# Optimization experiments

Hardware: AMD Instinct MI355X
Metric: run time of the kernel (lower is better)

The kernel has to match this reference:

```python
import jax, jax.numpy as jnp
import numpy as np

B, S = 8, 512          # batch, seq_len
D, F = 1024, 2048      # d_model, head hidden dim
H = 16                 # num_tasks (= num heads)
V = 3000               # selfies vocab
O = 1                  # head output size
INIT = 0.02


def setup_inputs() -> dict:
    key = jax.random.key(0)
    ks = jax.random.split(key, 12)
    return {
        "selfies": jax.random.randint(ks[0], (B, S), 0, V),
        "tasks": jax.random.randint(ks[1], (B, S), 0, H + 1),  # 0 -> invalid (-1)
        "values": jax.random.normal(ks[2], (B, S), jnp.float32),
        "property_mask": jax.random.randint(ks[3], (B, S), 0, 2).astype(bool),
        # shared_base params (embed + FFN -> [B,S,D])
        "emb_selfies": jax.random.normal(ks[4], (V, D), jnp.float32) * INIT,
        "emb_tasks": jax.random.normal(ks[5], (H + 1, D), jnp.float32) * INIT,
        "val_vec": jax.random.normal(ks[6], (D,), jnp.float32) * INIT,
        "Ws": jax.random.normal(ks[7], (D, D), jnp.float32) * INIT,
        "bs": jnp.zeros((D,), jnp.float32),
        # stacked per-head MLP params: Linear(D,F) -> GELU -> Linear(F,O)
        "W1": jax.random.normal(ks[8], (H, D, F), jnp.float32) * INIT,
        "b1": jnp.zeros((H, F), jnp.float32),
        "W2": jax.random.normal(ks[9], (H, F, O), jnp.float32) * INIT,
        "b2": jnp.zeros((H, O), jnp.float32),
    }


def reference(selfies, tasks, values, property_mask,
              emb_selfies, emb_tasks, val_vec, Ws, bs, W1, b1, W2, b2):
    # ---- shared_base: embed + masked token features + FFN -> [B,S,D] ----
    h = (emb_selfies[selfies] + emb_tasks[tasks] + values[..., None] * val_vec)
    h = h * property_mask[..., None].astype(h.dtype)
    shared = jax.nn.gelu(h @ Ws + bs)                      # [B,S,D]

    # ---- routing: task token -> head index, 0 means invalid (-1) ----
    head_idx = jnp.where(tasks > 0, (tasks - 1) % H, -1)   # [B,S]

    # ---- each active head runs its MLP over the FULL shared_output ----
    hid = jax.nn.gelu(jnp.einsum('bsd,hdf->bshf', shared, W1) + b1)  # [B,S,H,F]
    heads_out = jnp.einsum('bshf,hfo->bsho', hid, W2) + b2           # [B,S,H,O]

    # ---- scatter/select per token by head index; invalid -> zeros ----
    idx = jnp.clip(head_idx, 0)
    out = jnp.take_along_axis(heads_out, idx[..., None, None], axis=2)[:, :, 0, :]
    return jnp.where(head_idx[..., None] >= 0, out, jnp.zeros_like(out))
```

## Files before the change

### kernel.cpp

```cpp
#include <hip/hip_runtime.h>
#include <hip/hip_bf16.h>

#define TOK 4096
#define DD  1024
#define FF  2048
#define NH  16

typedef short bf16x8 __attribute__((ext_vector_type(8)));
typedef float f32x4  __attribute__((ext_vector_type(4)));

__device__ __forceinline__ float gelu_f(float x) {
  float u = 0.7978845608028654f * (x + 0.044715f * x * x * x);
  float e = __expf(2.0f * u);
  return 0.5f * x * (2.0f - 2.0f / (e + 1.0f));
}

__device__ __forceinline__ unsigned short f2bf(float f) {
  union { float f; unsigned u; } v; v.f = f;
  unsigned r = v.u + 0x7FFF + ((v.u >> 16) & 1);
  return (unsigned short)(r >> 16);
}
__device__ __forceinline__ unsigned pack2(float a, float b) {
  return (unsigned)f2bf(a) | ((unsigned)f2bf(b) << 16);
}

__device__ __forceinline__ void load_lds16(const void* g, void* l) {
  __builtin_amdgcn_global_load_lds(
      (const __attribute__((address_space(1))) void*)g,
      (__attribute__((address_space(3))) void*)l, 16, 0, 0);
}

__device__ __forceinline__ void wtile_convert(
    const float* __restrict__ src, int stride,
    unsigned short* __restrict__ dstBase, int nt0, int kc0,
    unsigned short (*T)[70]) {
  const int tid = threadIdx.x;
  {
    int r = tid >> 2, cq = (tid & 3) * 16;
    const float* p = src + (size_t)r * stride + cq;
#pragma unroll
    for (int i = 0; i < 4; ++i) {
      float4 v = *(const float4*)(p + i * 4);
      *(unsigned*)&T[r][cq + i * 4 + 0] = pack2(v.x, v.y);
      *(unsigned*)&T[r][cq + i * 4 + 2] = pack2(v.z, v.w);
    }
  }
  __syncthreads();
#pragma unroll
  for (int cc = 0; cc < 2; ++cc) {
    int idx = tid + cc * 256;
    int lane2 = idx & 63, kcl = (idx >> 6) & 1, ntl = idx >> 7;
    int n_local = ntl * 16 + (lane2 & 15);
    int r0 = kcl * 32 + (lane2 >> 4) * 8;
    unsigned short e[8];
#pragma unroll
    for (int j = 0; j < 8; ++j) e[j] = T[r0 + j][n_local];
    uint4 o;
    o.x = (unsigned)e[0] | ((unsigned)e[1] << 16);
    o.y = (unsigned)e[2] | ((unsigned)e[3] << 16);
    o.z = (unsigned)e[4] | ((unsigned)e[5] << 16);
    o.w = (unsigned)e[6] | ((unsigned)e[7] << 16);
    size_t chunk = ((size_t)(nt0 + ntl) * 32 + (kc0 + kcl)) * 64 + lane2;
    *(uint4*)(dstBase + chunk * 8) = o;
  }
}

#define WS_BLKS 256
#define PX_BLKS (TOK * 128 / 256)

__global__ __launch_bounds__(256) void prep_small(
    const int* __restrict__ selfies, const int* __restrict__ tasks,
    const float* __restrict__ values, const int* __restrict__ pmask,
    const float* __restrict__ emb_s, const float* __restrict__ emb_t,
    const float* __restrict__ val_vec, const float* __restrict__ Ws,
    const float* __restrict__ b2,
    unsigned short* __restrict__ Xb, unsigned short* __restrict__ Wsp,
    int* __restrict__ counts, int* __restrict__ lists, float* __restrict__ out) {
  __shared__ unsigned short T[64][70];
  int bid = blockIdx.x;
  if (bid < WS_BLKS) {
    int fb = bid & 15, kb = bid >> 4;
    wtile_convert(Ws + (size_t)(kb * 64) * DD + fb * 64, DD, Wsp,
                  fb * 4, kb * 2, T);
  } else if (bid < WS_BLKS + PX_BLKS) {
    int gid = (bid - WS_BLKS) * 256 + threadIdx.x;
    int kc = (gid & 127) * 8;
    int t  = gid >> 7;
    int sid = selfies[t], tsk = tasks[t];
    float v = values[t];
    float msk = pmask[t] ? 1.0f : 0.0f;
    const float* ps = emb_s + (size_t)sid * DD + kc;
    const float* pt = emb_t + (size_t)tsk * DD + kc;
    const float* pv = val_vec + kc;
    float r[8];
#pragma unroll
    for (int j = 0; j < 8; j += 4) {
      float4 a = *(const float4*)(ps + j);
      float4 b = *(const float4*)(pt + j);
      float4 c = *(const float4*)(pv + j);
      r[j + 0] = (a.x + b.x + v * c.x) * msk;
      r[j + 1] = (a.y + b.y + v * c.y) * msk;
      r[j + 2] = (a.z + b.z + v * c.z) * msk;
      r[j + 3] = (a.w + b.w + v * c.w) * msk;
    }
    uint4 o;
    o.x = pack2(r[0], r[1]); o.y = pack2(r[2], r[3]);
    o.z = pack2(r[4], r[5]); o.w = pack2(r[6], r[7]);
    *(uint4*)(Xb + (size_t)gid * 8) = o;
  } else {
    int t = (bid - WS_BLKS - PX_BLKS) * 256 + threadIdx.x;
    if (t < TOK) {
      int task = tasks[t];
      if (task > 0) {
        int h = (task - 1) & (NH - 1);
        int pos = atomicAdd(&counts[h], 1);
        lists[h * TOK + pos] = t;
        out[t] = b2[h];
      } else {
        out[t] = 0.0f;
      }
    }
  }
}

#define G1_BLKS  512
#define W1_BLKS  (16 * 16 * 32)

__device__ void gemm1_body(
    int bid, const unsigned short* __restrict__ Xb,
    const unsigned short* __restrict__ Wsp, const float* __restrict__ bs,
    unsigned short* __restrict__ shared_bf, char* smem) {
  unsigned short* As = (unsigned short*)smem;
  unsigned short* Bs = (unsigned short*)(smem + 16384);

  const int tid = threadIdx.x;
  const int lane = tid & 63, w = tid >> 6;
  const int m0 = (bid & 63) * 64;
  const int n0 = (bid >> 6) * 128;
  const int q = lane >> 4, c = lane & 15;

  const unsigned short* aSrc = Xb + (size_t)(m0 + w * 16 + c) * DD + q * 8;
  const unsigned short* bBase =
      Wsp + ((size_t)((bid >> 6) * 8 + w * 2)) * 32 * 512 + lane * 8;
  f32x4 acc[4][2] = {};

  float bsv[2];
  bsv[0] = bs[n0 + w * 32 + c];
  bsv[1] = bs[n0 + w * 32 + 16 + c];
  asm volatile("" :: "v"(bsv[0]), "v"(bsv[1]));

  auto stage = [&](int buf, int kc2) {
    load_lds16(aSrc + kc2 * 32, As + buf * 2048 + (size_t)(w * 64 + lane) * 8);
    const unsigned short* bk = bBase + kc2 * 512;
    load_lds16(bk,         Bs + buf * 4096 + (size_t)((w * 2 + 0) * 64 + lane) * 8);
    load_lds16(bk + 16384, Bs + buf * 4096 + (size_t)((w * 2 + 1) * 64 + lane) * 8);
  };
  auto compute = [&](int buf) {
    bf16x8 a[4], b[2];
#pragma unroll
    for (int mt = 0; mt < 4; ++mt)
      a[mt] = *(const bf16x8*)(As + buf * 2048 + (size_t)(mt * 64 + lane) * 8);
#pragma unroll
    for (int t = 0; t < 2; ++t)
      b[t] = *(const bf16x8*)(Bs + buf * 4096 + (size_t)((w * 2 + t) * 64 + lane) * 8);
    __builtin_amdgcn_s_setprio(1);
#pragma unroll
    for (int mt = 0; mt < 4; ++mt)
#pragma unroll
      for (int t = 0; t < 2; ++t)
        acc[mt][t] = __builtin_amdgcn_mfma_f32_16x16x32_bf16(a[mt], b[t], acc[mt][t], 0, 0, 0);
    __builtin_amdgcn_s_setprio(0);
  };

  stage(0, 0);
  stage(1, 1);
  for (int i = 0; i < 30; ++i) {
    stage((i + 2) & 3, i + 2);
    asm volatile("s_waitcnt vmcnt(6)" ::: "memory");
    __builtin_amdgcn_s_barrier();
    compute(i & 3);
    asm volatile("" ::: "memory");
  }
  asm volatile("s_waitcnt vmcnt(3)" ::: "memory");
  __builtin_amdgcn_s_barrier();
  compute(2);
  asm volatile("" ::: "memory");
  asm volatile("s_waitcnt vmcnt(0)" ::: "memory");
  __builtin_amdgcn_s_barrier();
  compute(3);

#pragma unroll
  for (int mt = 0; mt < 4; ++mt)
#pragma unroll
    for (int t = 0; t < 2; ++t)
#pragma unroll
      for (int r = 0; r < 4; ++r) {
        int row = m0 + mt * 16 + q * 4 + r;
        int col = n0 + w * 32 + t * 16 + c;
        shared_bf[(size_t)row * DD + col] = f2bf(gelu_f(acc[mt][t][r] + bsv[t]));
      }
}

__global__ __launch_bounds__(256) void gemm1_w1prep(
    const unsigned short* __restrict__ Xb, const unsigned short* __restrict__ Wsp,
    const float* __restrict__ bs, unsigned short* __restrict__ shared_bf,
    const float* __restrict__ W1, unsigned short* __restrict__ W1p) {
  __shared__ __align__(16) char smem[49152];
  int bid = blockIdx.x;
  if (bid < G1_BLKS) {
    gemm1_body(bid, Xb, Wsp, bs, shared_bf, smem);
  } else {
    int b = bid - G1_BLKS;
    int fb = b & 31, kb = (b >> 5) & 15, h = b >> 9;
    wtile_convert(W1 + ((size_t)h * DD + kb * 64) * FF + fb * 64, FF, W1p,
                  h * 128 + fb * 4, kb * 2,
                  (unsigned short (*)[70])smem);
  }
}

__global__ __launch_bounds__(512) void gemm2_mfma(
    const unsigned short* __restrict__ shared_bf, const unsigned short* __restrict__ W1p,
    const float* __restrict__ b1, const float* __restrict__ W2,
    const int* __restrict__ counts, const int* __restrict__ lists,
    float* __restrict__ out) {
  const int id = blockIdx.x;
  const int xcd = id & 7, local_ = id >> 3;
  const int h = xcd + 8 * (local_ >> 7);
  const int rest = local_ & 127;
  const int fc = rest & 15;
  const int m0 = (rest >> 4) * 64;
  const int nt_h = counts[h];
  if (m0 >= nt_h) return;

  __shared__ __align__(16) unsigned short As[4][4 * 64 * 8];
  __shared__ __align__(16) unsigned short Bs[4][8 * 64 * 8];
  __shared__ int   stok[64];
  __shared__ float red[8][68];

  const int tid = threadIdx.x;
  const int lane = tid & 63, w = tid >> 6;
  const int q = lane >> 4, c = lane & 15;

  if (tid < 64) {
    int i = m0 + tid;
    stok[tid] = (i < nt_h) ? lists[h * TOK + i] : -1;
  }
  __syncthreads();

  int tokr = stok[(w & 3) * 16 + c];
  if (tokr < 0) tokr = 0;
  const unsigned short* aSrc = shared_bf + (size_t)tokr * DD + q * 8;
  const unsigned short* bBase =
      W1p + ((size_t)h * 128 + fc * 8 + w) * 32 * 512 + lane * 8;

  f32x4 acc[4] = {};

  float b1v = b1[(size_t)h * FF + fc * 128 + w * 16 + c];
  float w2v = W2[(size_t)h * FF + fc * 128 + w * 16 + c];
  asm volatile("" :: "v"(b1v), "v"(w2v));

  const bool loadsA = (w < 4);

  auto stage = [&](int buf, int kc2) {
    if (loadsA)
      load_lds16(aSrc + kc2 * 32, As[buf] + (size_t)(w * 64 + lane) * 8);
    load_lds16(bBase + kc2 * 512, Bs[buf] + (size_t)(w * 64 + lane) * 8);
  };
  auto compute = [&](int buf) {
    bf16x8 a[4], b;
#pragma unroll
    for (int mt = 0; mt < 4; ++mt)
      a[mt] = *(const bf16x8*)(As[buf] + (size_t)(mt * 64 + lane) * 8);
    b = *(const bf16x8*)(Bs[buf] + (size_t)(w * 64 + lane) * 8);
    __builtin_amdgcn_s_setprio(1);
#pragma unroll
    for (int mt = 0; mt < 4; ++mt)
      acc[mt] = __builtin_amdgcn_mfma_f32_16x16x32_bf16(a[mt], b, acc[mt], 0, 0, 0);
    __builtin_amdgcn_s_setprio(0);
  };

  stage(0, 0);
  stage(1, 1);
  for (int i = 0; i < 30; ++i) {
    stage((i + 2) & 3, i + 2);
    if (loadsA) { asm volatile("s_waitcnt vmcnt(4)" ::: "memory"); }
    else        { asm volatile("s_waitcnt vmcnt(2)" ::: "memory"); }
    __builtin_amdgcn_s_barrier();
    compute(i & 3);
    asm volatile("" ::: "memory");
  }
  if (loadsA) { asm volatile("s_waitcnt vmcnt(2)" ::: "memory"); }
  else        { asm volatile("s_waitcnt vmcnt(1)" ::: "memory"); }
  __builtin_amdgcn_s_barrier();
  compute(2);
  asm volatile("" ::: "memory");
  asm volatile("s_waitcnt vmcnt(0)" ::: "memory");
  __builtin_amdgcn_s_barrier();
  compute(3);

#pragma unroll
  for (int mt = 0; mt < 4; ++mt)
#pragma unroll
    for (int r = 0; r < 4; ++r) {
      float s = gelu_f(acc[mt][r] + b1v) * w2v;
      s += __shfl_xor(s, 1);
      s += __shfl_xor(s, 2);
      s += __shfl_xor(s, 4);
      s += __shfl_xor(s, 8);
      if (c == 0) red[w][mt * 16 + q * 4 + r] = s;
    }
  __syncthreads();

  if (tid < 64) {
    int t = stok[tid];
    if (t >= 0) {
      float s = 0.0f;
#pragma unroll
      for (int ww = 0; ww < 8; ++ww) s += red[ww][tid];
      atomicAdd(&out[t], s);
    }
  }
}

extern "C" void kernel_launch(void* const* d_in, const int* in_sizes, int n_in,
                              void* d_out, int out_size, void* d_ws, size_t ws_size,
                              hipStream_t stream) {
  const int*   selfies = (const int*)d_in[0];
  const int*   tasks   = (const int*)d_in[1];
  const float* values  = (const float*)d_in[2];
  const int*   pmask   = (const int*)d_in[3];
  const float* emb_s   = (const float*)d_in[4];
  const float* emb_t   = (const float*)d_in[5];
  const float* val_vec = (const float*)d_in[6];
  const float* Ws      = (const float*)d_in[7];
  const float* bs      = (const float*)d_in[8];
  const float* W1      = (const float*)d_in[9];
  const float* b1      = (const float*)d_in[10];
  const float* W2      = (const float*)d_in[11];
  const float* b2      = (const float*)d_in[12];
  float* out = (float*)d_out;

  char* ws = (char*)d_ws;
  unsigned short* Xb        = (unsigned short*)ws;
  unsigned short* shared_bf = (unsigned short*)(ws + (8u << 20));
  unsigned short* Wsp       = (unsigned short*)(ws + (16u << 20));
  unsigned short* W1p       = (unsigned short*)(ws + (18u << 20));
  int* counts = (int*)(ws + (82u << 20));
  int* lists  = (int*)(ws + (82u << 20) + 256);

  hipMemsetAsync(counts, 0, NH * sizeof(int), stream);
  prep_small<<<WS_BLKS + PX_BLKS + TOK / 256, 256, 0, stream>>>(
      selfies, tasks, values, pmask, emb_s, emb_t, val_vec, Ws, b2,
      Xb, Wsp, counts, lists, out);
  gemm1_w1prep<<<G1_BLKS + W1_BLKS, 256, 0, stream>>>(
      Xb, Wsp, bs, shared_bf, W1, W1p);
  gemm2_mfma<<<2048, 512, 0, stream>>>(shared_bf, W1p, b1, W2,
                                       counts, lists, out);
}
```

Baseline: 302.2 us.

## Move W1 bf16 conversion into prep kernel with fp32-staged 32x128 tiles

The W1 fp32-to-bf16 repacking moves out of the kernel it shared with gemm1 and into the first prep kernel, using a new 32x128 tile converter that stages fp32 in LDS and packs only when writing out. gemm1 then runs as its own kernel with a 2D grid and its own LDS. The aim is to stop the large W1 conversion from competing with gemm1 and to give the conversion a wider, simpler access pattern. The cost is that the conversion can no longer overlap with gemm1, so the prep kernel grows into the critical path.

```diff
diff --git a/kernel.cpp b/kernel.cpp
--- a/kernel.cpp
+++ b/kernel.cpp
@@ -30,7 +30,42 @@
       (__attribute__((address_space(3))) void*)l, 16, 0, 0);
 }
 
-__device__ __forceinline__ void wtile_convert(
+#define W1C_BLKS 8192
+#define WS_BLKS  256
+#define PX_BLKS  (TOK * 128 / 256)
+#define RT_BLKS  (TOK / 256)
+
+__device__ void w1conv_body(int b, const float* __restrict__ W1,
+                            unsigned short* __restrict__ W1p,
+                            float (*Tf)[132]) {
+  int fb = b & 15, kb = (b >> 4) & 31, h = b >> 9;
+  const float* src = W1 + ((size_t)h * DD + kb * 32) * FF + fb * 128;
+  const int tid = threadIdx.x;
+  int row = tid >> 5, col4 = (tid & 31) * 4;
+#pragma unroll
+  for (int p = 0; p < 4; ++p) {
+    float4 v = *(const float4*)(src + (size_t)(p * 8 + row) * FF + col4);
+    *(float4*)&Tf[p * 8 + row][col4] = v;
+  }
+  __syncthreads();
+  int nt0 = h * 128 + fb * 8;
+#pragma unroll
+  for (int cc = 0; cc < 2; ++cc) {
+    int idx = tid + cc * 256;
+    int lane2 = idx & 63, ntl = idx >> 6;
+    int nl = ntl * 16 + (lane2 & 15);
+    int r0 = (lane2 >> 4) * 8;
+    uint4 o;
+    o.x = pack2(Tf[r0 + 0][nl], Tf[r0 + 1][nl]);
+    o.y = pack2(Tf[r0 + 2][nl], Tf[r0 + 3][nl]);
+    o.z = pack2(Tf[r0 + 4][nl], Tf[r0 + 5][nl]);
+    o.w = pack2(Tf[r0 + 6][nl], Tf[r0 + 7][nl]);
+    size_t chunk = ((size_t)(nt0 + ntl) * 32 + kb) * 64 + lane2;
+    *(uint4*)(W1p + chunk * 8) = o;
+  }
+}
+
+__device__ void wtile_convert(
     const float* __restrict__ src, int stride,
     unsigned short* __restrict__ dstBase, int nt0, int kc0,
     unsigned short (*T)[70]) {
@@ -65,25 +100,26 @@
   }
 }
 
-#define WS_BLKS 256
-#define PX_BLKS (TOK * 128 / 256)
-
-__global__ __launch_bounds__(256) void prep_small(
+__global__ __launch_bounds__(256) void prep_all2(
     const int* __restrict__ selfies, const int* __restrict__ tasks,
     const float* __restrict__ values, const int* __restrict__ pmask,
     const float* __restrict__ emb_s, const float* __restrict__ emb_t,
     const float* __restrict__ val_vec, const float* __restrict__ Ws,
-    const float* __restrict__ b2,
+    const float* __restrict__ W1, const float* __restrict__ b2,
     unsigned short* __restrict__ Xb, unsigned short* __restrict__ Wsp,
+    unsigned short* __restrict__ W1p,
     int* __restrict__ counts, int* __restrict__ lists, float* __restrict__ out) {
-  __shared__ unsigned short T[64][70];
+  __shared__ __align__(16) char smem[32 * 132 * 4];
   int bid = blockIdx.x;
-  if (bid < WS_BLKS) {
-    int fb = bid & 15, kb = bid >> 4;
+  if (bid < W1C_BLKS) {
+    w1conv_body(bid, W1, W1p, (float (*)[132])smem);
+  } else if (bid < W1C_BLKS + WS_BLKS) {
+    int b2i = bid - W1C_BLKS;
+    int fb = b2i & 15, kb = b2i >> 4;
     wtile_convert(Ws + (size_t)(kb * 64) * DD + fb * 64, DD, Wsp,
-                  fb * 4, kb * 2, T);
-  } else if (bid < WS_BLKS + PX_BLKS) {
-    int gid = (bid - WS_BLKS) * 256 + threadIdx.x;
+                  fb * 4, kb * 2, (unsigned short (*)[70])smem);
+  } else if (bid < W1C_BLKS + WS_BLKS + PX_BLKS) {
+    int gid = (bid - W1C_BLKS - WS_BLKS) * 256 + threadIdx.x;
     int kc = (gid & 127) * 8;
     int t  = gid >> 7;
     int sid = selfies[t], tsk = tasks[t];
@@ -108,7 +144,7 @@
     o.z = pack2(r[4], r[5]); o.w = pack2(r[6], r[7]);
     *(uint4*)(Xb + (size_t)gid * 8) = o;
   } else {
-    int t = (bid - WS_BLKS - PX_BLKS) * 256 + threadIdx.x;
+    int t = (bid - W1C_BLKS - WS_BLKS - PX_BLKS) * 256 + threadIdx.x;
     if (t < TOK) {
       int task = tasks[t];
       if (task > 0) {
@@ -123,25 +159,20 @@
   }
 }
 
-#define G1_BLKS  512
-#define W1_BLKS  (16 * 16 * 32)
-
-__device__ void gemm1_body(
-    int bid, const unsigned short* __restrict__ Xb,
-    const unsigned short* __restrict__ Wsp, const float* __restrict__ bs,
-    unsigned short* __restrict__ shared_bf, char* smem) {
-  unsigned short* As = (unsigned short*)smem;
-  unsigned short* Bs = (unsigned short*)(smem + 16384);
+__global__ __launch_bounds__(256) void gemm1_mfma(
+    const unsigned short* __restrict__ Xb, const unsigned short* __restrict__ Wsp,
+    const float* __restrict__ bs, unsigned short* __restrict__ shared_bf) {
+  __shared__ __align__(16) unsigned short As[4][4 * 64 * 8];
+  __shared__ __align__(16) unsigned short Bs[4][8 * 64 * 8];
 
   const int tid = threadIdx.x;
   const int lane = tid & 63, w = tid >> 6;
-  const int m0 = (bid & 63) * 64;
-  const int n0 = (bid >> 6) * 128;
+  const int m0 = blockIdx.x * 64;
+  const int n0 = blockIdx.y * 128;
   const int q = lane >> 4, c = lane & 15;
 
   const unsigned short* aSrc = Xb + (size_t)(m0 + w * 16 + c) * DD + q * 8;
-  const unsigned short* bBase =
-      Wsp + ((size_t)((bid >> 6) * 8 + w * 2)) * 32 * 512 + lane * 8;
+  const unsigned short* bBase = Wsp + ((size_t)(blockIdx.y * 8 + w * 2)) * 32 * 512 + lane * 8;
   f32x4 acc[4][2] = {};
 
   float bsv[2];
@@ -150,19 +181,19 @@
   asm volatile("" :: "v"(bsv[0]), "v"(bsv[1]));
 
   auto stage = [&](int buf, int kc2) {
-    load_lds16(aSrc + kc2 * 32, As + buf * 2048 + (size_t)(w * 64 + lane) * 8);
+    load_lds16(aSrc + kc2 * 32, As[buf] + (size_t)(w * 64 + lane) * 8);
     const unsigned short* bk = bBase + kc2 * 512;
-    load_lds16(bk,         Bs + buf * 4096 + (size_t)((w * 2 + 0) * 64 + lane) * 8);
-    load_lds16(bk + 16384, Bs + buf * 4096 + (size_t)((w * 2 + 1) * 64 + lane) * 8);
+    load_lds16(bk,            Bs[buf] + (size_t)((w * 2 + 0) * 64 + lane) * 8);
+    load_lds16(bk + 16384,    Bs[buf] + (size_t)((w * 2 + 1) * 64 + lane) * 8);
   };
   auto compute = [&](int buf) {
     bf16x8 a[4], b[2];
 #pragma unroll
     for (int mt = 0; mt < 4; ++mt)
-      a[mt] = *(const bf16x8*)(As + buf * 2048 + (size_t)(mt * 64 + lane) * 8);
+      a[mt] = *(const bf16x8*)(As[buf] + (size_t)(mt * 64 + lane) * 8);
 #pragma unroll
     for (int t = 0; t < 2; ++t)
-      b[t] = *(const bf16x8*)(Bs + buf * 4096 + (size_t)((w * 2 + t) * 64 + lane) * 8);
+      b[t] = *(const bf16x8*)(Bs[buf] + (size_t)((w * 2 + t) * 64 + lane) * 8);
     __builtin_amdgcn_s_setprio(1);
 #pragma unroll
     for (int mt = 0; mt < 4; ++mt)
@@ -199,23 +230,6 @@
         int col = n0 + w * 32 + t * 16 + c;
         shared_bf[(size_t)row * DD + col] = f2bf(gelu_f(acc[mt][t][r] + bsv[t]));
       }
-}
-
-__global__ __launch_bounds__(256) void gemm1_w1prep(
-    const unsigned short* __restrict__ Xb, const unsigned short* __restrict__ Wsp,
-    const float* __restrict__ bs, unsigned short* __restrict__ shared_bf,
-    const float* __restrict__ W1, unsigned short* __restrict__ W1p) {
-  __shared__ __align__(16) char smem[49152];
-  int bid = blockIdx.x;
-  if (bid < G1_BLKS) {
-    gemm1_body(bid, Xb, Wsp, bs, shared_bf, smem);
-  } else {
-    int b = bid - G1_BLKS;
-    int fb = b & 31, kb = (b >> 5) & 15, h = b >> 9;
-    wtile_convert(W1 + ((size_t)h * DD + kb * 64) * FF + fb * 64, FF, W1p,
-                  h * 128 + fb * 4, kb * 2,
-                  (unsigned short (*)[70])smem);
-  }
 }
 
 __global__ __launch_bounds__(512) void gemm2_mfma(
@@ -349,11 +363,10 @@
   int* lists  = (int*)(ws + (82u << 20) + 256);
 
   hipMemsetAsync(counts, 0, NH * sizeof(int), stream);
-  prep_small<<<WS_BLKS + PX_BLKS + TOK / 256, 256, 0, stream>>>(
-      selfies, tasks, values, pmask, emb_s, emb_t, val_vec, Ws, b2,
-      Xb, Wsp, counts, lists, out);
-  gemm1_w1prep<<<G1_BLKS + W1_BLKS, 256, 0, stream>>>(
-      Xb, Wsp, bs, shared_bf, W1, W1p);
+  prep_all2<<<W1C_BLKS + WS_BLKS + PX_BLKS + RT_BLKS, 256, 0, stream>>>(
+      selfies, tasks, values, pmask, emb_s, emb_t, val_vec, Ws, W1, b2,
+      Xb, Wsp, W1p, counts, lists, out);
+  gemm1_mfma<<<dim3(TOK / 64, DD / 128), 256, 0, stream>>>(Xb, Wsp, bs, shared_bf);
   gemm2_mfma<<<2048, 512, 0, stream>>>(shared_bf, W1p, b1, W2,
                                        counts, lists, out);
 }
```

Measured after the change: 301.8 us. No clear change (-0.1%).
